# Optimization experiments

Measured on AMD Instinct MI355X. Metric: run time of the kernel, lower is better.

The kernel has to match this reference:

```python
import jax, jax.numpy as jnp
import numpy as np

B, H, L, C, KD, NS = 4, 1024, 8192, 1, 64, 8  # batch, d_model, seq_len, channels, kernel_dim, num_scales
DECAY_MIN, DECAY_MAX = 1.0, 4.0


def _interp_linear(x, scale):
    """F.interpolate(mode='linear', align_corners=False) for integer scale on last axis."""
    if scale == 1:
        return x
    Lin = x.shape[-1]
    Lout = Lin * scale
    pos = (jnp.arange(Lout, dtype=x.dtype) + 0.5) / scale - 0.5
    lo = jnp.floor(pos)
    w = pos - lo  # fractional weight toward hi
    lo_i = jnp.clip(lo.astype(jnp.int32), 0, Lin - 1)
    hi_i = jnp.clip(lo.astype(jnp.int32) + 1, 0, Lin - 1)
    return x[..., lo_i] * (1.0 - w) + x[..., hi_i] * w


def setup_inputs() -> dict:
    key = jax.random.key(0)
    k1, k2, k3, k4 = jax.random.split(key, 4)
    return {
        "u": jax.random.normal(k1, (B, H, L), jnp.float32),
        "kernels": jax.random.normal(k2, (NS, C, H, KD), jnp.float32),
        "D": jax.random.normal(k3, (C, H), jnp.float32),
        "W_out": jax.random.normal(k4, (H, C * H), jnp.float32) / np.sqrt(C * H).astype(np.float32),
        "b_out": jnp.zeros((H,), jnp.float32),
    }


def reference(u, kernels, D, W_out, b_out):
    # --- multi-scale kernel synthesis ('cat' mode, init_scale=0) ---
    mult = jnp.linspace(DECAY_MIN, DECAY_MAX, H).astype(u.dtype).reshape(1, H, 1)
    parts = [
        _interp_linear(kernels[i], 2 ** max(0, i - 1)) * mult ** (NS - 1 - i)
        for i in range(NS)
    ]
    k = jnp.concatenate(parts, axis=-1)  # (C, H, 8192) == (C, H, L) for these dims
    # kernel_norm is computed from the untruncated kernel and detached (buffer)
    knorm = jax.lax.stop_gradient(jnp.linalg.norm(k, axis=-1, keepdims=True))  # (C, H, 1)
    k = k[..., :L] / knorm

    # --- FFT long convolution (causal, via 2L-padded circular conv) ---
    n = 2 * L
    k_f = jnp.fft.rfft(k, n=n)                 # (C, H, L+1) complex
    u_f = jnp.fft.rfft(u, n=n)                 # (B, H, L+1) complex
    y = jnp.fft.irfft(u_f[:, None, :, :] * k_f[None, :, :, :], n=n)[..., :L]  # (B, C, H, L)
    y = y + jnp.einsum('bhl,ch->bchl', u, D)   # skip connection
    y = y.reshape(u.shape[0], C * H, L)        # (B, C*H, L)

    # --- activation + output linear (1x1 conv) ---
    y = jax.nn.gelu(y, approximate=False)      # torch nn.GELU is exact erf form
    y = jnp.einsum('oh,bhl->bol', W_out, y) + b_out[None, :, None]
    return y
```

## Files before the change

kernel.cpp:

```cpp
#include <hip/hip_runtime.h>
#include <hip/hip_bf16.h>

#define LFULL 8192
#define HDIM 1024
#define KPAD 8448
#define USTRIDE 8320
#define UCHUNKS 1040
#define CSTRIDE 1040

typedef __attribute__((ext_vector_type(8))) short bf16x8;
typedef __attribute__((ext_vector_type(4))) float f32x4;
typedef __attribute__((ext_vector_type(16))) float f32x16;

union U16 {
  uint4 u;
  bf16x8 s;
  ushort e[8];
};

__device__ __forceinline__ ushort f2bf(float x) {
  union { float f; uint u; } a;
  a.f = x;
  uint r = a.u + 0x7fffu + ((a.u >> 16) & 1u);
  return (ushort)(r >> 16);
}
__device__ __forceinline__ float bf2f(ushort x) {
  union { uint u; float f; } a;
  a.u = ((uint)x) << 16;
  return a.f;
}

__device__ __forceinline__ void gload16(const void* src, void* lds) {
  __builtin_amdgcn_global_load_lds(
      (const __attribute__((address_space(1))) unsigned int*)src,
      (__attribute__((address_space(3))) unsigned int*)lds, 16, 0, 0);
}

__device__ __forceinline__ uint ALIGNB(uint hi, uint lo, uint sh) {
#if __has_builtin(__builtin_amdgcn_alignbyte)
  return __builtin_amdgcn_alignbyte(hi, lo, sh);
#else
  return (uint)((((unsigned long long)hi << 32) | (unsigned long long)lo) >> (8u * sh));
#endif
}

#define USWZ16(cI) ((cI) ^ (((cI) >> 4) & 15))

__global__ __launch_bounds__(256) void k_synth_kernel(
    const float* __restrict__ kern, ushort* __restrict__ kout) {
  const int h = blockIdx.x;
  const int tid = threadIdx.x;
  __shared__ float Kw[8][64];
  __shared__ __align__(16) float kv[LFULL];
  __shared__ float red[8];
  for (int idx = tid; idx < 8 * 64; idx += 256) {
    int i = idx >> 6, j = idx & 63;
    Kw[i][j] = kern[(i * HDIM + h) * 64 + j];
  }
  __syncthreads();
  const float mult = (float)(1.0 + 3.0 * (double)h / 1023.0);
  float pw[8];
  pw[7] = 1.0f;
#pragma unroll
  for (int i = 6; i >= 0; --i) pw[i] = pw[i + 1] * mult;
  float ss = 0.0f;
  for (int m = tid; m < LFULL; m += 256) {
    const int i = (m < 64) ? 0 : (32 - __clz(m >> 6));
    const int slog = (i == 0) ? 0 : (i - 1);
    const float inv_s = 1.0f / (float)(1 << slog);
    const int off = (i == 0) ? 0 : (64 << (i - 1));
    const int t = m - off;
    const float pos = ((float)t + 0.5f) * inv_s - 0.5f;
    const float lof = floorf(pos);
    const float wgt = pos - lof;
    int lo = (int)lof;
    int hi = lo + 1;
    lo = min(63, max(0, lo));
    hi = min(63, max(0, hi));
    const float val = (Kw[i][lo] * (1.0f - wgt) + Kw[i][hi] * wgt) * pw[i];
    kv[m] = val;
    ss += val * val;
  }
#pragma unroll
  for (int o = 32; o > 0; o >>= 1) ss += __shfl_xor(ss, o, 64);
  if ((tid & 63) == 0) red[tid >> 6] = ss;
  __syncthreads();
  if (tid == 0) red[0] = sqrtf(red[0] + red[1] + red[2] + red[3]);
  __syncthreads();
  const float inv_norm = 1.0f / red[0];
  ushort* krow = kout + (size_t)h * KPAD;
  for (int m = tid; m < LFULL; m += 256) krow[8191 - m] = f2bf(kv[m] * inv_norm);
  if (tid < 256) krow[8192 + tid] = 0;
}

__global__ __launch_bounds__(256, 2) void conv_mfma_kernel(
    const float* __restrict__ u, const ushort* __restrict__ kbrev,
    const float* __restrict__ Dp, ushort* __restrict__ g) {
  __shared__ __align__(16) ushort Us[4 * USTRIDE];
  __shared__ __align__(16) ushort RingC[8 * 520];
  const int tid = threadIdx.x;
  const int h = blockIdx.x;
  const int w = tid >> 6;
  const int lane = tid & 63;
  const int c32 = lane & 31;
  const int qh = lane >> 5;
  uint4* Us4 = (uint4*)Us;
  char* ringB = (char*)RingC;
  const int wbase = w * UCHUNKS + 16;

  if (tid < 64) Us4[(tid >> 4) * UCHUNKS + (tid & 15)] = make_uint4(0, 0, 0, 0);
  for (int cc = tid; cc < 4096; cc += 256) {
    const int row = cc >> 10, cI = cc & 1023;
    const float* up = u + (((size_t)(row * HDIM + h)) << 13) + (cI << 3);
    const float4 v0 = *(const float4*)up;
    const float4 v1 = *(const float4*)(up + 4);
    U16 pk;
    pk.e[0] = f2bf(v0.x); pk.e[1] = f2bf(v0.y);
    pk.e[2] = f2bf(v0.z); pk.e[3] = f2bf(v0.w);
    pk.e[4] = f2bf(v1.x); pk.e[5] = f2bf(v1.y);
    pk.e[6] = f2bf(v1.z); pk.e[7] = f2bf(v1.w);
    Us4[(row * UCHUNKS + 16) + USWZ16(cI)] = pk.u;
  }

  const ushort* kr = kbrev + (size_t)h * KPAD;
  char* ringE = ringB + (2 * w) * CSTRIDE;
  char* ringO = ringB + (2 * w + 1) * CSTRIDE;
#pragma unroll
  for (int cn = 62; cn <= 64; ++cn) {
    const int x0 = 128 * cn + 2 * lane;
    const uint kEp = *(const uint*)(kr + x0);
    const uint kMp = *(const uint*)(kr + x0 - 2);
    const int off = (2 * x0 + 4 * w) & 1023;
    *(uint*)(ringE + off) = kEp;
    *(uint*)(ringO + off) = ALIGNB(kEp, kMp, 2);
  }
  uint kE = *(const uint*)(kr + 61 * 128 + 2 * lane);
  uint kM = *(const uint*)(kr + 61 * 128 + 2 * lane - 2);
  __syncthreads();

  f32x16 acc[2][4];
#pragma unroll
  for (int f = 0; f < 2; ++f)
#pragma unroll
    for (int rg = 0; rg < 4; ++rg)
#pragma unroll
      for (int q = 0; q < 16; ++q) acc[f][rg][q] = 0.0f;

  const int PBASE = 8191 - c32 + 8 * qh;
  const int sph = (c32 + 1) & 7;
  const char* ringR = ringB + sph * CSTRIDE;
  int bd = 2 * (PBASE + sph) + 256;

  uint4 WA[8], WB[8];
#pragma unroll
  for (int i = 0; i < 8; ++i) WB[i] = make_uint4(0, 0, 0, 0);

#define FPART(DD, F, WFRESH, WCARR) {                                   \
    const int j0 = (F) * 32 + c32 - (DD);                               \
    const int jc = j0 < 0 ? -1 : j0;                                    \
    const int pb = jc << 4;                                             \
    const int px = jc & 15;                                             \
    _Pragma("unroll")                                                   \
    for (int ks = 0; ks < 8; ++ks) {                                    \
      const int t = 2 * ks + qh;                                        \
      U16 bb;                                                           \
      bb.u = Us4[wbase + pb + (t ^ px)];                                \
      U16 a0, a1, a2, a3;                                               \
      a0.u = (8 - ks >= 7) ? WFRESH[1 - ks] : WCARR[9 - ks];            \
      a1.u = (10 - ks >= 7) ? WFRESH[3 - ks] : WCARR[11 - ks];          \
      a2.u = (12 - ks >= 7) ? WFRESH[5 - ks] : WCARR[13 - ks];          \
      a3.u = WFRESH[7 - ks];                                            \
      acc[F][0] = __builtin_amdgcn_mfma_f32_32x32x16_bf16(a0.s, bb.s, acc[F][0], 0, 0, 0); \
      acc[F][1] = __builtin_amdgcn_mfma_f32_32x32x16_bf16(a1.s, bb.s, acc[F][1], 0, 0, 0); \
      acc[F][2] = __builtin_amdgcn_mfma_f32_32x32x16_bf16(a2.s, bb.s, acc[F][2], 0, 0, 0); \
      acc[F][3] = __builtin_amdgcn_mfma_f32_32x32x16_bf16(a3.s, bb.s, acc[F][3], 0, 0, 0); \
    } }

#define STEP(DD, WFRESH, WCARR, HASF0) {                                \
    const int cw = (61 - (DD)) < 0 ? 0 : (61 - (DD));                   \
    const int offw = (((cw & 3) << 8) + 4 * lane + 4 * w) & 1023;       \
    *(uint*)(ringE + offw) = kE;                                        \
    *(uint*)(ringO + offw) = ALIGNB(kE, kM, 2);                         \
    const int cn = (60 - (DD)) < 0 ? 0 : (60 - (DD));                   \
    const uint kE2 = *(const uint*)(kr + cn * 128 + 2 * lane);          \
    const uint kM2 = *(const uint*)(kr + cn * 128 + 2 * lane - 2);      \
    _Pragma("unroll")                                                   \
    for (int i = 0; i < 8; ++i) {                                       \
      const int off = (bd - 224 - 32 * i) & 1023;                       \
      WFRESH[i] = *(const uint4*)(ringR + off);                         \
    }                                                                   \
    if (HASF0) { FPART(DD, 0, WFRESH, WCARR); FPART(DD, 1, WFRESH, WCARR); } \
    else { FPART(DD, 1, WFRESH, WCARR); }                               \
    kE = kE2; kM = kM2;                                                 \
    bd -= 256;                                                          \
    asm volatile("s_waitcnt lgkmcnt(0)" ::: "memory");                  \
    __builtin_amdgcn_s_barrier();                                       \
    __builtin_amdgcn_sched_barrier(0);                                  \
  }

  for (int dd = 0; dd < 32; dd += 2) {
    STEP(dd, WA, WB, true);
    STEP(dd + 1, WB, WA, true);
  }
  for (int dd = 32; dd < 64; dd += 2) {
    STEP(dd, WA, WB, false);
    STEP(dd + 1, WB, WA, false);
  }

  const float Dh = Dp[h];
  ushort* gp = g + (((size_t)(w * HDIM + h)) << 13);
  const ushort* urow = Us + w * USTRIDE + 128;
#pragma unroll
  for (int f = 0; f < 2; ++f) {
#pragma unroll
    for (int rg = 0; rg < 4; ++rg) {
      const int lbase = (f * 32 + c32) * 128 + rg * 32 + 4 * qh;
#pragma unroll
      for (int rq = 0; rq < 4; ++rq) {
        const int l = lbase + 8 * rq;
        const int cI = l >> 3;
        const int phys = USWZ16(cI);
        const uint2 uv = *(const uint2*)(urow + (phys << 3) + 4 * qh);
        float uu[4];
        uu[0] = bf2f((ushort)(uv.x & 0xffff));
        uu[1] = bf2f((ushort)(uv.x >> 16));
        uu[2] = bf2f((ushort)(uv.y & 0xffff));
        uu[3] = bf2f((ushort)(uv.y >> 16));
        ushort o[4];
#pragma unroll
        for (int jj = 0; jj < 4; ++jj) {
          const float y = acc[f][rg][rq * 4 + jj] + Dh * uu[jj];
          const float ge = 0.5f * y * (1.0f + erff(y * 0.70710678118654752f));
          o[jj] = f2bf(ge);
        }
        uint2 op;
        op.x = (uint)o[0] | ((uint)o[1] << 16);
        op.y = (uint)o[2] | ((uint)o[3] << 16);
        *(uint2*)(gp + l) = op;
      }
    }
  }
}

__global__ __launch_bounds__(256) void transpose_kernel(
    const ushort* __restrict__ g, ushort* __restrict__ gt) {
  __shared__ __align__(16) ushort Ts[64 * 64];
  const int l0 = blockIdx.x * 64, hh0 = blockIdx.y * 64, b = blockIdx.z;
  const int tid = threadIdx.x;
#pragma unroll
  for (int p = 0; p < 2; ++p) {
    const int hh = (tid >> 3) + 32 * p;
    const int c8 = tid & 7;
    const uint4 v = *(const uint4*)(g + (((size_t)(b * HDIM + hh0 + hh)) << 13)
                                    + l0 + c8 * 8);
    ((uint4*)Ts)[hh * 8 + (c8 ^ ((hh >> 3) & 7))] = v;
  }
  __syncthreads();
#pragma unroll
  for (int p = 0; p < 2; ++p) {
    const int lr = (tid >> 3) + 32 * p;
    const int o8 = tid & 7;
    U16 pk;
#pragma unroll
    for (int j = 0; j < 8; ++j) {
      const int hq = o8 * 8 + j;
      pk.e[j] = Ts[hq * 64 + (((lr >> 3) ^ o8) << 3) + (lr & 7)];
    }
    ((uint4*)(gt + ((size_t)b * LFULL + l0 + lr) * HDIM + hh0))[o8] = pk.u;
  }
}

__global__ __launch_bounds__(256) void wcvt_kernel(const float* __restrict__ W,
                                                   ushort* __restrict__ Wb) {
  const int i = (blockIdx.x * 256 + threadIdx.x) * 8;
  const float4 v0 = *(const float4*)(W + i);
  const float4 v1 = *(const float4*)(W + i + 4);
  U16 pk;
  pk.e[0] = f2bf(v0.x); pk.e[1] = f2bf(v0.y);
  pk.e[2] = f2bf(v0.z); pk.e[3] = f2bf(v0.w);
  pk.e[4] = f2bf(v1.x); pk.e[5] = f2bf(v1.y);
  pk.e[6] = f2bf(v1.z); pk.e[7] = f2bf(v1.w);
  ((uint4*)Wb)[i >> 3] = pk.u;
}

__global__ __launch_bounds__(256, 2) void outmm_kernel(
    const ushort* __restrict__ Wb, const ushort* __restrict__ gt,
    const float* __restrict__ bo, float* __restrict__ out) {
  __shared__ __align__(16) ushort As[128 * 32];
  __shared__ __align__(16) ushort Bs[128 * 32];
  const int tid = threadIdx.x;
  const int l0 = blockIdx.x * 128, o0 = blockIdx.y * 128, b = blockIdx.z;
  const int w = tid >> 6, lane = tid & 63;
  const int wm = w >> 1, wn = w & 1;
  const int col = lane & 15, q = lane >> 4;
  const int srow = lane >> 2, scol = (lane & 3) * 8;
  f32x4 acc[4][4];
#pragma unroll
  for (int m = 0; m < 4; ++m)
#pragma unroll
    for (int n = 0; n < 4; ++n) acc[m][n] = (f32x4){0.f, 0.f, 0.f, 0.f};
  const ushort* gb = gt + ((size_t)b * LFULL) * HDIM;
  for (int kt = 0; kt < 32; ++kt) {
    const int k0 = kt * 32;
    const int r0 = w * 32;
#pragma unroll
    for (int ii = 0; ii < 2; ++ii) {
      const int ra = r0 + ii * 16 + srow;
      gload16(Wb + (size_t)(o0 + ra) * HDIM + k0 + scol,
              As + (r0 + ii * 16) * 32);
      gload16(gb + (size_t)(l0 + ra) * HDIM + k0 + scol,
              Bs + (r0 + ii * 16) * 32);
    }
    __syncthreads();
    bf16x8 aa[4], bb[4];
#pragma unroll
    for (int m = 0; m < 4; ++m) {
      aa[m] = ((const bf16x8*)As)[(wm * 64 + m * 16 + col) * 4 + q];
      bb[m] = ((const bf16x8*)Bs)[(wn * 64 + m * 16 + col) * 4 + q];
    }
#pragma unroll
    for (int m = 0; m < 4; ++m)
#pragma unroll
      for (int n = 0; n < 4; ++n)
        acc[m][n] = __builtin_amdgcn_mfma_f32_16x16x32_bf16(aa[m], bb[n],
                                                            acc[m][n], 0, 0, 0);
    __syncthreads();
  }
#pragma unroll
  for (int m = 0; m < 4; ++m) {
    const int ob = o0 + wm * 64 + m * 16 + q * 4;
    const float4 bv = *(const float4*)(bo + ob);
    const float bva[4] = {bv.x, bv.y, bv.z, bv.w};
#pragma unroll
    for (int n = 0; n < 4; ++n) {
      const int l = l0 + wn * 64 + n * 16 + col;
      float* op = out + (((size_t)(b * HDIM + ob)) << 13) + l;
#pragma unroll
      for (int v = 0; v < 4; ++v) op[(size_t)v << 13] = acc[m][n][v] + bva[v];
    }
  }
}

extern "C" void kernel_launch(void* const* d_in, const int* in_sizes, int n_in,
                              void* d_out, int out_size, void* d_ws,
                              size_t ws_size, hipStream_t stream) {
  const float* u = (const float*)d_in[0];
  const float* kern = (const float*)d_in[1];
  const float* D = (const float*)d_in[2];
  const float* W = (const float*)d_in[3];
  const float* bo = (const float*)d_in[4];
  float* out = (float*)d_out;

  char* ws = (char*)d_ws;
  ushort* g = (ushort*)ws;
  ushort* gt = (ushort*)(ws + ((size_t)64 << 20));
  ushort* kbrev = (ushort*)(ws + ((size_t)128 << 20));
  ushort* Wb = (ushort*)(ws + ((size_t)128 << 20));

  k_synth_kernel<<<HDIM, 256, 0, stream>>>(kern, kbrev);
  conv_mfma_kernel<<<HDIM, 256, 0, stream>>>(u, kbrev, D, g);
  wcvt_kernel<<<512, 256, 0, stream>>>(W, Wb);
  transpose_kernel<<<dim3(128, 16, 4), 256, 0, stream>>>(g, gt);
  outmm_kernel<<<dim3(64, 8, 4), 256, 0, stream>>>(Wb, gt, bo, out);
}
```

Before: 464.0 us.

## Split conv blocks across batch pairs and row-group halves for occupancy

The conv kernel now launches two blocks per channel, each handling two batch rows. Within a block, two waves share a batch row and each takes half of the row groups, so a wave holds 4 accumulators instead of 8. LDS use for the input drops by half and launch bounds rise to 3 blocks per CU, aiming for more parallelism and latency hiding. In exchange, each block recomputes the kernel ring loads for the same h, so kernel-ring traffic and setup per output roughly double.

```diff
diff --git a/kernel.cpp b/kernel.cpp
--- a/kernel.cpp
+++ b/kernel.cpp
@@ -93,25 +93,29 @@
   if (tid < 256) krow[8192 + tid] = 0;
 }
 
-__global__ __launch_bounds__(256, 2) void conv_mfma_kernel(
+__global__ __launch_bounds__(256, 3) void conv_mfma_kernel(
     const float* __restrict__ u, const ushort* __restrict__ kbrev,
     const float* __restrict__ Dp, ushort* __restrict__ g) {
-  __shared__ __align__(16) ushort Us[4 * USTRIDE];
+  __shared__ __align__(16) ushort Us[2 * USTRIDE];
   __shared__ __align__(16) ushort RingC[8 * 520];
   const int tid = threadIdx.x;
-  const int h = blockIdx.x;
+  const int h = blockIdx.x >> 1;
+  const int bp = blockIdx.x & 1;
   const int w = tid >> 6;
+  const int bl = w >> 1;
+  const int ch = w & 1;
   const int lane = tid & 63;
   const int c32 = lane & 31;
   const int qh = lane >> 5;
   uint4* Us4 = (uint4*)Us;
   char* ringB = (char*)RingC;
-  const int wbase = w * UCHUNKS + 16;
-
-  if (tid < 64) Us4[(tid >> 4) * UCHUNKS + (tid & 15)] = make_uint4(0, 0, 0, 0);
-  for (int cc = tid; cc < 4096; cc += 256) {
+  const int wbase = bl * UCHUNKS + 16;
+
+  if (tid < 32) Us4[(tid >> 4) * UCHUNKS + (tid & 15)] = make_uint4(0, 0, 0, 0);
+  for (int cc = tid; cc < 2048; cc += 256) {
     const int row = cc >> 10, cI = cc & 1023;
-    const float* up = u + (((size_t)(row * HDIM + h)) << 13) + (cI << 3);
+    const float* up =
+        u + (((size_t)((bp * 2 + row) * HDIM + h)) << 13) + (cI << 3);
     const float4 v0 = *(const float4*)up;
     const float4 v1 = *(const float4*)(up + 4);
     U16 pk;
@@ -138,11 +142,11 @@
   uint kM = *(const uint*)(kr + 61 * 128 + 2 * lane - 2);
   __syncthreads();
 
-  f32x16 acc[2][4];
+  f32x16 acc[2][2];
 #pragma unroll
   for (int f = 0; f < 2; ++f)
 #pragma unroll
-    for (int rg = 0; rg < 4; ++rg)
+    for (int rg = 0; rg < 2; ++rg)
 #pragma unroll
       for (int q = 0; q < 16; ++q) acc[f][rg][q] = 0.0f;
 
@@ -155,7 +159,9 @@
 #pragma unroll
   for (int i = 0; i < 8; ++i) WB[i] = make_uint4(0, 0, 0, 0);
 
-#define FPART(DD, F, WFRESH, WCARR) {                                   \
+#define WGETX(WFRESH, WCARR, MM) ((MM) >= 7 ? (WFRESH)[(MM)-7] : (WCARR)[(MM)+1])
+
+#define FPART(DD, F, WFRESH, WCARR, W0B, W1B) {                         \
     const int j0 = (F) * 32 + c32 - (DD);                               \
     const int jc = j0 < 0 ? -1 : j0;                                    \
     const int pb = jc << 4;                                             \
@@ -165,18 +171,14 @@
       const int t = 2 * ks + qh;                                        \
       U16 bb;                                                           \
       bb.u = Us4[wbase + pb + (t ^ px)];                                \
-      U16 a0, a1, a2, a3;                                               \
-      a0.u = (8 - ks >= 7) ? WFRESH[1 - ks] : WCARR[9 - ks];            \
-      a1.u = (10 - ks >= 7) ? WFRESH[3 - ks] : WCARR[11 - ks];          \
-      a2.u = (12 - ks >= 7) ? WFRESH[5 - ks] : WCARR[13 - ks];          \
-      a3.u = WFRESH[7 - ks];                                            \
+      U16 a0, a1;                                                       \
+      a0.u = WGETX(WFRESH, WCARR, (W0B) - ks);                          \
+      a1.u = WGETX(WFRESH, WCARR, (W1B) - ks);                          \
       acc[F][0] = __builtin_amdgcn_mfma_f32_32x32x16_bf16(a0.s, bb.s, acc[F][0], 0, 0, 0); \
       acc[F][1] = __builtin_amdgcn_mfma_f32_32x32x16_bf16(a1.s, bb.s, acc[F][1], 0, 0, 0); \
-      acc[F][2] = __builtin_amdgcn_mfma_f32_32x32x16_bf16(a2.s, bb.s, acc[F][2], 0, 0, 0); \
-      acc[F][3] = __builtin_amdgcn_mfma_f32_32x32x16_bf16(a3.s, bb.s, acc[F][3], 0, 0, 0); \
     } }
 
-#define STEP(DD, WFRESH, WCARR, HASF0) {                                \
+#define STEP(DD, WFRESH, WCARR, HASF0, W0B, W1B) {                      \
     const int cw = (61 - (DD)) < 0 ? 0 : (61 - (DD));                   \
     const int offw = (((cw & 3) << 8) + 4 * lane + 4 * w) & 1023;       \
     *(uint*)(ringE + offw) = kE;                                        \
@@ -189,8 +191,12 @@
       const int off = (bd - 224 - 32 * i) & 1023;                       \
       WFRESH[i] = *(const uint4*)(ringR + off);                         \
     }                                                                   \
-    if (HASF0) { FPART(DD, 0, WFRESH, WCARR); FPART(DD, 1, WFRESH, WCARR); } \
-    else { FPART(DD, 1, WFRESH, WCARR); }                               \
+    if (HASF0) {                                                        \
+      FPART(DD, 0, WFRESH, WCARR, W0B, W1B);                            \
+      FPART(DD, 1, WFRESH, WCARR, W0B, W1B);                            \
+    } else {                                                            \
+      FPART(DD, 1, WFRESH, WCARR, W0B, W1B);                            \
+    }                                                                   \
     kE = kE2; kM = kM2;                                                 \
     bd -= 256;                                                          \
     asm volatile("s_waitcnt lgkmcnt(0)" ::: "memory");                  \
@@ -198,22 +204,35 @@
     __builtin_amdgcn_sched_barrier(0);                                  \
   }
 
-  for (int dd = 0; dd < 32; dd += 2) {
-    STEP(dd, WA, WB, true);
-    STEP(dd + 1, WB, WA, true);
-  }
-  for (int dd = 32; dd < 64; dd += 2) {
-    STEP(dd, WA, WB, false);
-    STEP(dd + 1, WB, WA, false);
+  if (ch == 0) {
+    for (int dd = 0; dd < 32; dd += 2) {
+      STEP(dd, WA, WB, true, 8, 10);
+      STEP(dd + 1, WB, WA, true, 8, 10);
+    }
+    for (int dd = 32; dd < 64; dd += 2) {
+      STEP(dd, WA, WB, false, 8, 10);
+      STEP(dd + 1, WB, WA, false, 8, 10);
+    }
+  } else {
+    for (int dd = 0; dd < 32; dd += 2) {
+      STEP(dd, WA, WB, true, 12, 14);
+      STEP(dd + 1, WB, WA, true, 12, 14);
+    }
+    for (int dd = 32; dd < 64; dd += 2) {
+      STEP(dd, WA, WB, false, 12, 14);
+      STEP(dd + 1, WB, WA, false, 12, 14);
+    }
   }
 
   const float Dh = Dp[h];
-  ushort* gp = g + (((size_t)(w * HDIM + h)) << 13);
-  const ushort* urow = Us + w * USTRIDE + 128;
+  const int b = bp * 2 + bl;
+  ushort* gp = g + (((size_t)(b * HDIM + h)) << 13);
+  const ushort* urow = Us + bl * USTRIDE + 128;
 #pragma unroll
   for (int f = 0; f < 2; ++f) {
 #pragma unroll
-    for (int rg = 0; rg < 4; ++rg) {
+    for (int rgl = 0; rgl < 2; ++rgl) {
+      const int rg = 2 * ch + rgl;
       const int lbase = (f * 32 + c32) * 128 + rg * 32 + 4 * qh;
 #pragma unroll
       for (int rq = 0; rq < 4; ++rq) {
@@ -229,7 +248,7 @@
         ushort o[4];
 #pragma unroll
         for (int jj = 0; jj < 4; ++jj) {
-          const float y = acc[f][rg][rq * 4 + jj] + Dh * uu[jj];
+          const float y = acc[f][rgl][rq * 4 + jj] + Dh * uu[jj];
           const float ge = 0.5f * y * (1.0f + erff(y * 0.70710678118654752f));
           o[jj] = f2bf(ge);
         }
@@ -358,7 +377,7 @@
   ushort* Wb = (ushort*)(ws + ((size_t)128 << 20));
 
   k_synth_kernel<<<HDIM, 256, 0, stream>>>(kern, kbrev);
-  conv_mfma_kernel<<<HDIM, 256, 0, stream>>>(u, kbrev, D, g);
+  conv_mfma_kernel<<<2 * HDIM, 256, 0, stream>>>(u, kbrev, D, g);
   wcvt_kernel<<<512, 256, 0, stream>>>(W, Wb);
   transpose_kernel<<<dim3(128, 16, 4), 256, 0, stream>>>(g, gt);
   outmm_kernel<<<dim3(64, 8, 4), 256, 0, stream>>>(Wb, gt, bo, out);
```

New measurement: 529.4 us. 14.1% more time.

## Restructure kernel ring buffer to four wave copies and barrier every two steps

Applied to the files above, without the earlier changes.

The conv kernel's shared-memory ring that stages the reversed filter is rebuilt. It drops from eight even/odd-shifted copies to four per-wave copies, each shifted by the wave index, with a deeper 8-chunk window and a wraparound guard. Reads now use two 8-byte loads instead of one 16-byte load, so the alignbyte shuffles are gone. The workgroup barrier runs every other step instead of every step, which cuts synchronisation overhead but relies on the larger ring to avoid read/write hazards. The misaligned 8-byte LDS reads may cost bandwidth or cause bank conflicts.

```diff
diff --git a/kernel.cpp b/kernel.cpp
--- a/kernel.cpp
+++ b/kernel.cpp
@@ -6,7 +6,7 @@
 #define KPAD 8448
 #define USTRIDE 8320
 #define UCHUNKS 1040
-#define CSTRIDE 1040
+#define CSTR2 2080
 
 typedef __attribute__((ext_vector_type(8))) short bf16x8;
 typedef __attribute__((ext_vector_type(4))) float f32x4;
@@ -34,14 +34,6 @@
   __builtin_amdgcn_global_load_lds(
       (const __attribute__((address_space(1))) unsigned int*)src,
       (__attribute__((address_space(3))) unsigned int*)lds, 16, 0, 0);
-}
-
-__device__ __forceinline__ uint ALIGNB(uint hi, uint lo, uint sh) {
-#if __has_builtin(__builtin_amdgcn_alignbyte)
-  return __builtin_amdgcn_alignbyte(hi, lo, sh);
-#else
-  return (uint)((((unsigned long long)hi << 32) | (unsigned long long)lo) >> (8u * sh));
-#endif
 }
 
 #define USWZ16(cI) ((cI) ^ (((cI) >> 4) & 15))
@@ -97,7 +89,7 @@
     const float* __restrict__ u, const ushort* __restrict__ kbrev,
     const float* __restrict__ Dp, ushort* __restrict__ g) {
   __shared__ __align__(16) ushort Us[4 * USTRIDE];
-  __shared__ __align__(16) ushort RingC[8 * 520];
+  __shared__ __align__(16) ushort RingC[4 * (CSTR2 / 2)];
   const int tid = threadIdx.x;
   const int h = blockIdx.x;
   const int w = tid >> 6;
@@ -123,19 +115,15 @@
   }
 
   const ushort* kr = kbrev + (size_t)h * KPAD;
-  char* ringE = ringB + (2 * w) * CSTRIDE;
-  char* ringO = ringB + (2 * w + 1) * CSTRIDE;
-#pragma unroll
-  for (int cn = 62; cn <= 64; ++cn) {
-    const int x0 = 128 * cn + 2 * lane;
-    const uint kEp = *(const uint*)(kr + x0);
-    const uint kMp = *(const uint*)(kr + x0 - 2);
-    const int off = (2 * x0 + 4 * w) & 1023;
-    *(uint*)(ringE + off) = kEp;
-    *(uint*)(ringO + off) = ALIGNB(kEp, kMp, 2);
-  }
-  uint kE = *(const uint*)(kr + 61 * 128 + 2 * lane);
-  uint kM = *(const uint*)(kr + 61 * 128 + 2 * lane - 2);
+  char* ringW = ringB + w * CSTR2;
+#pragma unroll
+  for (int cn = 59; cn <= 65; ++cn) {
+    const uint kv = *(const uint*)(kr + cn * 128 + 2 * lane - 4 * w);
+    const int offw = (256 * cn + 4 * lane) & 2047;
+    *(uint*)(ringW + offw) = kv;
+    if (offw < 16) *(uint*)(ringW + offw + 2048) = kv;
+  }
+  uint kreg = *(const uint*)(kr + 58 * 128 + 2 * lane - 4 * w);
   __syncthreads();
 
   f32x16 acc[2][4];
@@ -147,13 +135,19 @@
       for (int q = 0; q < 16; ++q) acc[f][rg][q] = 0.0f;
 
   const int PBASE = 8191 - c32 + 8 * qh;
-  const int sph = (c32 + 1) & 7;
-  const char* ringR = ringB + sph * CSTRIDE;
-  int bd = 2 * (PBASE + sph) + 256;
+  const int cpy = (c32 + 1) & 3;
+  const char* ringR = ringB + cpy * CSTR2;
+  int BD = 2 * (PBASE + 16 + 4 * cpy);
 
   uint4 WA[8], WB[8];
 #pragma unroll
   for (int i = 0; i < 8; ++i) WB[i] = make_uint4(0, 0, 0, 0);
+
+#define RD_W(i, DST) {                                                  \
+    const int a_ = (BD - 32 * (i)) & 2047;                              \
+    const uint2 lo_ = *(const uint2*)(ringR + a_);                      \
+    const uint2 hi_ = *(const uint2*)(ringR + a_ + 8);                  \
+    (DST) = make_uint4(lo_.x, lo_.y, hi_.x, hi_.y); }
 
 #define FPART(DD, F, WFRESH, WCARR) {                                   \
     const int j0 = (F) * 32 + c32 - (DD);                               \
@@ -176,35 +170,34 @@
       acc[F][3] = __builtin_amdgcn_mfma_f32_32x32x16_bf16(a3.s, bb.s, acc[F][3], 0, 0, 0); \
     } }
 
-#define STEP(DD, WFRESH, WCARR, HASF0) {                                \
-    const int cw = (61 - (DD)) < 0 ? 0 : (61 - (DD));                   \
-    const int offw = (((cw & 3) << 8) + 4 * lane + 4 * w) & 1023;       \
-    *(uint*)(ringE + offw) = kE;                                        \
-    *(uint*)(ringO + offw) = ALIGNB(kE, kM, 2);                         \
-    const int cn = (60 - (DD)) < 0 ? 0 : (60 - (DD));                   \
-    const uint kE2 = *(const uint*)(kr + cn * 128 + 2 * lane);          \
-    const uint kM2 = *(const uint*)(kr + cn * 128 + 2 * lane - 2);      \
+#define STEP(DD, WFRESH, WCARR, HASF0, DOSYNC) {                        \
     _Pragma("unroll")                                                   \
-    for (int i = 0; i < 8; ++i) {                                       \
-      const int off = (bd - 224 - 32 * i) & 1023;                       \
-      WFRESH[i] = *(const uint4*)(ringR + off);                         \
+    for (int i = 0; i < 8; ++i) RD_W(i, WFRESH[i]);                     \
+    {                                                                   \
+      const int cw = (58 - (DD)) < 0 ? 0 : (58 - (DD));                 \
+      const int offw = (((cw & 7) << 8) + 4 * lane) & 2047;             \
+      *(uint*)(ringW + offw) = kreg;                                    \
+      if (offw < 16) *(uint*)(ringW + offw + 2048) = kreg;              \
+      const int cn = (57 - (DD)) < 0 ? 0 : (57 - (DD));                 \
+      kreg = *(const uint*)(kr + cn * 128 + 2 * lane - 4 * w);          \
     }                                                                   \
     if (HASF0) { FPART(DD, 0, WFRESH, WCARR); FPART(DD, 1, WFRESH, WCARR); } \
     else { FPART(DD, 1, WFRESH, WCARR); }                               \
-    kE = kE2; kM = kM2;                                                 \
-    bd -= 256;                                                          \
-    asm volatile("s_waitcnt lgkmcnt(0)" ::: "memory");                  \
-    __builtin_amdgcn_s_barrier();                                       \
-    __builtin_amdgcn_sched_barrier(0);                                  \
+    BD -= 256;                                                          \
+    if (DOSYNC) {                                                       \
+      asm volatile("s_waitcnt lgkmcnt(0)" ::: "memory");                \
+      __builtin_amdgcn_s_barrier();                                     \
+      __builtin_amdgcn_sched_barrier(0);                                \
+    }                                                                   \
   }
 
   for (int dd = 0; dd < 32; dd += 2) {
-    STEP(dd, WA, WB, true);
-    STEP(dd + 1, WB, WA, true);
+    STEP(dd, WA, WB, true, false);
+    STEP(dd + 1, WB, WA, true, true);
   }
   for (int dd = 32; dd < 64; dd += 2) {
-    STEP(dd, WA, WB, false);
-    STEP(dd + 1, WB, WA, false);
+    STEP(dd, WA, WB, false, false);
+    STEP(dd + 1, WB, WA, false, true);
   }
 
   const float Dh = Dp[h];
```

New measurement: 779.6 us. 68.0% more time.

## Double K-tile depth in output GEMM and XOR-swizzle LDS layout

Applied to the files above, without the earlier changes.

The output projection GEMM now stages a K-depth of 64 instead of 32 per iteration, halving the number of barrier pairs and load rounds. The LDS tiles are written with an XOR swizzle on 16-byte chunks, keyed by row, so that MFMA fragment reads spread across banks. The cost is doubled LDS per block, which may affect occupancy at two blocks per CU, and extra index arithmetic.

```diff
diff --git a/kernel.cpp b/kernel.cpp
--- a/kernel.cpp
+++ b/kernel.cpp
@@ -286,44 +286,51 @@
 __global__ __launch_bounds__(256, 2) void outmm_kernel(
     const ushort* __restrict__ Wb, const ushort* __restrict__ gt,
     const float* __restrict__ bo, float* __restrict__ out) {
-  __shared__ __align__(16) ushort As[128 * 32];
-  __shared__ __align__(16) ushort Bs[128 * 32];
+  __shared__ __align__(16) ushort As[128 * 64];
+  __shared__ __align__(16) ushort Bs[128 * 64];
   const int tid = threadIdx.x;
   const int l0 = blockIdx.x * 128, o0 = blockIdx.y * 128, b = blockIdx.z;
   const int w = tid >> 6, lane = tid & 63;
   const int wm = w >> 1, wn = w & 1;
   const int col = lane & 15, q = lane >> 4;
-  const int srow = lane >> 2, scol = (lane & 3) * 8;
+  const int srow = tid >> 3;
+  const int sch = tid & 7;
+  const int gch = sch ^ (srow & 7);
   f32x4 acc[4][4];
 #pragma unroll
   for (int m = 0; m < 4; ++m)
 #pragma unroll
     for (int n = 0; n < 4; ++n) acc[m][n] = (f32x4){0.f, 0.f, 0.f, 0.f};
   const ushort* gb = gt + ((size_t)b * LFULL) * HDIM;
-  for (int kt = 0; kt < 32; ++kt) {
-    const int k0 = kt * 32;
-    const int r0 = w * 32;
-#pragma unroll
-    for (int ii = 0; ii < 2; ++ii) {
-      const int ra = r0 + ii * 16 + srow;
-      gload16(Wb + (size_t)(o0 + ra) * HDIM + k0 + scol,
-              As + (r0 + ii * 16) * 32);
-      gload16(gb + (size_t)(l0 + ra) * HDIM + k0 + scol,
-              Bs + (r0 + ii * 16) * 32);
+  for (int kt = 0; kt < 16; ++kt) {
+    const int k0 = kt * 64;
+#pragma unroll
+    for (int ii = 0; ii < 4; ++ii) {
+      const int row = srow + 32 * ii;
+      gload16(Wb + (size_t)(o0 + row) * HDIM + k0 + gch * 8,
+              As + row * 64 + sch * 8);
+      gload16(gb + (size_t)(l0 + row) * HDIM + k0 + gch * 8,
+              Bs + row * 64 + sch * 8);
     }
     __syncthreads();
-    bf16x8 aa[4], bb[4];
-#pragma unroll
-    for (int m = 0; m < 4; ++m) {
-      aa[m] = ((const bf16x8*)As)[(wm * 64 + m * 16 + col) * 4 + q];
-      bb[m] = ((const bf16x8*)Bs)[(wn * 64 + m * 16 + col) * 4 + q];
-    }
-#pragma unroll
-    for (int m = 0; m < 4; ++m)
-#pragma unroll
-      for (int n = 0; n < 4; ++n)
-        acc[m][n] = __builtin_amdgcn_mfma_f32_16x16x32_bf16(aa[m], bb[n],
-                                                            acc[m][n], 0, 0, 0);
+    bf16x8 aa[2][4], bb[2][4];
+#pragma unroll
+    for (int kk = 0; kk < 2; ++kk)
+#pragma unroll
+      for (int m = 0; m < 4; ++m) {
+        const int ra = wm * 64 + m * 16 + col;
+        const int rb = wn * 64 + m * 16 + col;
+        aa[kk][m] = ((const bf16x8*)As)[ra * 8 + ((kk * 4 + q) ^ (ra & 7))];
+        bb[kk][m] = ((const bf16x8*)Bs)[rb * 8 + ((kk * 4 + q) ^ (rb & 7))];
+      }
+#pragma unroll
+    for (int kk = 0; kk < 2; ++kk)
+#pragma unroll
+      for (int m = 0; m < 4; ++m)
+#pragma unroll
+        for (int n = 0; n < 4; ++n)
+          acc[m][n] = __builtin_amdgcn_mfma_f32_16x16x32_bf16(
+              aa[kk][m], bb[kk][n], acc[m][n], 0, 0, 0);
     __syncthreads();
   }
 #pragma unroll
```

Measured after the change: 461.7 us. No clear change (-0.5%).
